# Kernel optimization log

Hardware: AMD Instinct MI355X
Metric: run time of the kernel (lower is better)

The kernel has to match this reference:

```python
import jax, jax.numpy as jnp
import numpy as np

N, E, D, H, G = 20000, 640000, 128, 128, 256  # nodes, edges, in_dim, hidden, num_graphs


def _xavier(k, shp):
    lim = float(np.sqrt(6.0 / (shp[0] + shp[1])))
    return jax.random.uniform(k, shp, jnp.float32, -lim, lim)


def setup_inputs() -> dict:
    key = jax.random.key(0)
    ks = jax.random.split(key, 16)
    x = jax.random.normal(ks[0], (N, D), jnp.float32)
    edge_index = jax.random.randint(ks[1], (2, E), 0, N)
    batch = jnp.sort(jax.random.randint(ks[2], (N,), 0, G))
    inp = {"x": x, "edge_index": edge_index, "batch": batch}
    dims = [(D, H), (H, H), (H, H)]
    ki = 3
    for i, (din, dh) in enumerate(dims):  # GIN MLP per layer: Linear-ReLU-Linear
        inp[f"w1_{i}"] = _xavier(ks[ki], (din, dh)); ki += 1
        inp[f"b1_{i}"] = jnp.zeros((dh,), jnp.float32)
        inp[f"w2_{i}"] = _xavier(ks[ki], (dh, dh)); ki += 1
        inp[f"b2_{i}"] = jnp.zeros((dh,), jnp.float32)
    inp["head_w1"] = _xavier(ks[ki], (H, H // 2)); ki += 1
    inp["head_b1"] = jnp.zeros((H // 2,), jnp.float32)
    inp["head_w2"] = _xavier(ks[ki], (H // 2, 1))
    inp["head_b2"] = jnp.zeros((1,), jnp.float32)
    return inp


def reference(x, edge_index, batch,
              w1_0, b1_0, w2_0, b2_0,
              w1_1, b1_1, w2_1, b2_1,
              w1_2, b1_2, w2_2, b2_2,
              head_w1, head_b1, head_w2, head_b2):
    src, dst = edge_index[0], edge_index[1]
    layers = [(w1_0, b1_0, w2_0, b2_0), (w1_1, b1_1, w2_1, b2_1), (w1_2, b1_2, w2_2, b2_2)]
    h = x
    for w1, b1, w2, b2 in layers:
        # GINConv (eps=0): aggregate neighbor sum + self, then MLP
        agg = jax.ops.segment_sum(h[src], dst, num_segments=N)  # [N, d] scatter-add
        z = agg + h
        z = jnp.maximum(z @ w1 + b1, 0.0) @ w2 + b2
        h = jnp.maximum(z, 0.0)  # ReLU after conv
    # global_mean_pool over graph ids
    sums = jax.ops.segment_sum(h, batch, num_segments=G)            # [G, H]
    counts = jax.ops.segment_sum(jnp.ones((N,), h.dtype), batch, num_segments=G)
    pooled = sums / jnp.maximum(counts, 1.0)[:, None]
    # head: Linear-ReLU-(Dropout eval=identity)-Linear
    hid = jnp.maximum(pooled @ head_w1 + head_b1, 0.0)
    return hid @ head_w2 + head_b2  # [G, 1]
```

## Files before the change

kernel.cpp:

```cpp
#include <hip/hip_runtime.h>


#define FEAT 128
#define CAP 128
#define SPILLCAP 4096

typedef unsigned short u16;
typedef unsigned int u32;
typedef __attribute__((ext_vector_type(8))) short bf16x8;
typedef __attribute__((ext_vector_type(4))) float f32x4;

__device__ __forceinline__ u32 f2bf(float f) {
    u32 u = __float_as_uint(f);
    return (u + 0x7FFFu + ((u >> 16) & 1u)) >> 16;
}
__device__ __forceinline__ float bf2f(u32 u) { return __uint_as_float(u << 16); }
__device__ __forceinline__ float bflo(u32 u) { return __uint_as_float(u << 16); }
__device__ __forceinline__ float bfhi(u32 u) { return __uint_as_float(u & 0xFFFF0000u); }

__device__ __forceinline__ void add8(uint4 v, float* a) {
    a[0] += bflo(v.x); a[1] += bfhi(v.x);
    a[2] += bflo(v.y); a[3] += bfhi(v.y);
    a[4] += bflo(v.z); a[5] += bfhi(v.z);
    a[6] += bflo(v.w); a[7] += bfhi(v.w);
}

__global__ __launch_bounds__(256) void cvt_x_kernel(
    const float* __restrict__ x, u16* __restrict__ xb, int total4,
    int* __restrict__ cnt, int n, int* __restrict__ spillCnt)
{
    int i = blockIdx.x * 256 + threadIdx.x;
    if (i < n) cnt[i] = 0;
    if (i == 0) *spillCnt = 0;
    if (i >= total4) return;
    float4 v = reinterpret_cast<const float4*>(x)[i];
    u32 lo = f2bf(v.x) | (f2bf(v.y) << 16);
    u32 hi = f2bf(v.z) | (f2bf(v.w) << 16);
    reinterpret_cast<uint2*>(xb)[i] = make_uint2(lo, hi);
}

struct WSet { const float* w[6]; };
__global__ __launch_bounds__(256) void cvt_wt_bounds_kernel(
    WSet ws, u16* __restrict__ outHi, u16* __restrict__ outLo,
    const int* __restrict__ batch, int* __restrict__ bnd, int n, int G)
{
    if (blockIdx.y == 6) {
        int g = blockIdx.x * 256 + threadIdx.x;
        if (g > G) return;
        int lo = 0, hi = n;
        while (lo < hi) {
            int mid = (lo + hi) >> 1;
            if (batch[mid] < g) lo = mid + 1; else hi = mid;
        }
        bnd[g] = lo;
        return;
    }
    int mat = blockIdx.y;
    const float* W = ws.w[mat];
    int i = blockIdx.x * 256 + threadIdx.x;
    int nn = i >> 7, k = i & 127;
    float f = W[(size_t)k * FEAT + nn];
    u32 hi = f2bf(f);
    u32 lo = f2bf(f - bf2f(hi));
    size_t o = (size_t)mat * FEAT * FEAT + (size_t)nn * FEAT + k;
    outHi[o] = (u16)hi;
    outLo[o] = (u16)lo;
}

__global__ __launch_bounds__(256) void csort_bucket_kernel(
    const int* __restrict__ src, const int* __restrict__ dst,
    int* __restrict__ cnt, u16* __restrict__ esrc,
    int* __restrict__ spillCnt, int2* __restrict__ spill, int nE)
{
    int e4 = (blockIdx.x * 256 + threadIdx.x) * 4;
    if (e4 + 3 < nE) {
        int4 d = *reinterpret_cast<const int4*>(&dst[e4]);
        int4 sv = *reinterpret_cast<const int4*>(&src[e4]);
        int p0 = atomicAdd(&cnt[d.x], 1);
        int p1 = atomicAdd(&cnt[d.y], 1);
        int p2 = atomicAdd(&cnt[d.z], 1);
        int p3 = atomicAdd(&cnt[d.w], 1);
        if (p0 < CAP) esrc[(size_t)d.x * CAP + p0] = (u16)sv.x;
        else { int q = atomicAdd(spillCnt, 1); if (q < SPILLCAP) spill[q] = make_int2(d.x, sv.x); }
        if (p1 < CAP) esrc[(size_t)d.y * CAP + p1] = (u16)sv.y;
        else { int q = atomicAdd(spillCnt, 1); if (q < SPILLCAP) spill[q] = make_int2(d.y, sv.y); }
        if (p2 < CAP) esrc[(size_t)d.z * CAP + p2] = (u16)sv.z;
        else { int q = atomicAdd(spillCnt, 1); if (q < SPILLCAP) spill[q] = make_int2(d.z, sv.z); }
        if (p3 < CAP) esrc[(size_t)d.w * CAP + p3] = (u16)sv.w;
        else { int q = atomicAdd(spillCnt, 1); if (q < SPILLCAP) spill[q] = make_int2(d.w, sv.w); }
    } else {
        for (int e = e4; e < nE; ++e) {
            int d = dst[e], s = src[e];
            int p = atomicAdd(&cnt[d], 1);
            if (p < CAP) esrc[(size_t)d * CAP + p] = (u16)s;
            else { int q = atomicAdd(spillCnt, 1); if (q < SPILLCAP) spill[q] = make_int2(d, s); }
        }
    }
}

__global__ __launch_bounds__(1024) void gin_layer_kernel(
    const u16* __restrict__ hin, const int* __restrict__ cnt,
    const u16* __restrict__ esrc,
    const int* __restrict__ spillCnt, const int2* __restrict__ spill,
    const u16* __restrict__ W1h, const u16* __restrict__ W1l,
    const float* __restrict__ B1,
    const u16* __restrict__ W2h, const u16* __restrict__ W2l,
    const float* __restrict__ B2,
    u16* __restrict__ out, int n)
{
    __shared__ float z_lds[4][16][132];
    __shared__ u16 thi_lds[16 * FEAT];
    __shared__ u16 tlo_lds[16 * FEAT];

    int tid = threadIdx.x;
    int rowBase = blockIdx.x * 16;

    {
        int nr = tid >> 6;
        int grp = (tid >> 4) & 3;
        int lane = tid & 15;
        int node = rowBase + nr;
        const uint4* h4 = reinterpret_cast<const uint4*>(hin);
        float a[8] = {0.f, 0.f, 0.f, 0.f, 0.f, 0.f, 0.f, 0.f};
        if (grp == 0) {
            uint4 u = h4[(size_t)node * 16 + lane];
            add8(u, a);
        }
        int len = cnt[node];
        if (len > CAP) len = CAP;
        int base = node * CAP;
        int qlen = (len + 3) >> 2;
        int gbeg = grp * qlen;
        int gend = min(gbeg + qlen, len);
        for (int j = gbeg; j < gend; j += 8) {
            uint4 v[8];
#pragma unroll
            for (int q = 0; q < 8; ++q) {
                int jj = j + q;
                int jc = jj < gend ? jj : (gend - 1);
                v[q] = h4[(size_t)esrc[base + jc] * 16 + lane];
                u32 m = (jj < gend) ? 0xFFFFFFFFu : 0u;
                v[q].x &= m; v[q].y &= m; v[q].z &= m; v[q].w &= m;
            }
#pragma unroll
            for (int q = 0; q < 8; ++q) add8(v[q], a);
        }
        if (grp == 0) {
            int sc = *spillCnt;
            if (sc > SPILLCAP) sc = SPILLCAP;
            for (int i = 0; i < sc; ++i) {
                int2 e = spill[i];
                if (e.x == node) {
                    uint4 v = h4[(size_t)e.y * 16 + lane];
                    add8(v, a);
                }
            }
        }
        *reinterpret_cast<float4*>(&z_lds[grp][nr][lane * 8]) =
            make_float4(a[0], a[1], a[2], a[3]);
        *reinterpret_cast<float4*>(&z_lds[grp][nr][lane * 8 + 4]) =
            make_float4(a[4], a[5], a[6], a[7]);
    }

    __syncthreads();

    int w = tid >> 6;
    int l = tid & 63;
    int l16 = l & 15;
    int lq = l >> 4;

    bf16x8 ah[4], al[4];
    f32x4 acc = (f32x4){0.f, 0.f, 0.f, 0.f};

    if (w < 8) {
#pragma unroll
        for (int q = 0; q < 4; ++q) {
            int off = q * 32 + lq * 8;
            float fv[8];
#pragma unroll
            for (int i = 0; i < 8; ++i) fv[i] = 0.0f;
#pragma unroll
            for (int g = 0; g < 4; ++g) {
                const float* zr = &z_lds[g][l16][off];
                float4 f0 = *reinterpret_cast<const float4*>(zr);
                float4 f1 = *reinterpret_cast<const float4*>(zr + 4);
                fv[0] += f0.x; fv[1] += f0.y; fv[2] += f0.z; fv[3] += f0.w;
                fv[4] += f1.x; fv[5] += f1.y; fv[6] += f1.z; fv[7] += f1.w;
            }
            bf16x8 hv, lv;
#pragma unroll
            for (int i = 0; i < 8; ++i) {
                u32 hb = f2bf(fv[i]);
                u32 lb = f2bf(fv[i] - bf2f(hb));
                hv[i] = (short)hb; lv[i] = (short)lb;
            }
            ah[q] = hv; al[q] = lv;
        }

        {
            const bf16x8* WrowH = reinterpret_cast<const bf16x8*>(W1h + (size_t)(w * 16 + l16) * FEAT);
            const bf16x8* WrowL = reinterpret_cast<const bf16x8*>(W1l + (size_t)(w * 16 + l16) * FEAT);
#pragma unroll
            for (int q = 0; q < 4; ++q) {
                bf16x8 wh = WrowH[q * 4 + lq];
                bf16x8 wl = WrowL[q * 4 + lq];
                acc = __builtin_amdgcn_mfma_f32_16x16x32_bf16(ah[q], wh, acc, 0, 0, 0);
                acc = __builtin_amdgcn_mfma_f32_16x16x32_bf16(al[q], wh, acc, 0, 0, 0);
                acc = __builtin_amdgcn_mfma_f32_16x16x32_bf16(ah[q], wl, acc, 0, 0, 0);
            }
        }

        {
            int col = w * 16 + l16;
            float bias = B1[col];
            int base16 = (w * 32) + ((l16 & 8) << 1);
            int fine = (l16 & 7) << 1;
#pragma unroll
            for (int r = 0; r < 4; ++r) {
                int rt = lq * 4 + r;
                float v = fmaxf(acc[r] + bias, 0.0f);
                u32 hi = f2bf(v);
                u32 lo = f2bf(v - bf2f(hi));
                int idx = (rt * 256 + ((base16 ^ (rt << 4)) | fine)) >> 1;
                thi_lds[idx] = (u16)hi;
                tlo_lds[idx] = (u16)lo;
            }
        }
    }

    __syncthreads();

    if (w < 8) {
        const bf16x8* thb = reinterpret_cast<const bf16x8*>(thi_lds);
        const bf16x8* tlb = reinterpret_cast<const bf16x8*>(tlo_lds);
        bf16x8 a2h[4], a2l[4];
#pragma unroll
        for (int q = 0; q < 4; ++q) {
            int idx = l16 * 16 + ((q * 4 + lq) ^ l16);
            a2h[q] = thb[idx];
            a2l[q] = tlb[idx];
        }

        acc = (f32x4){0.f, 0.f, 0.f, 0.f};

        {
            const bf16x8* WrowH = reinterpret_cast<const bf16x8*>(W2h + (size_t)(w * 16 + l16) * FEAT);
            const bf16x8* WrowL = reinterpret_cast<const bf16x8*>(W2l + (size_t)(w * 16 + l16) * FEAT);
#pragma unroll
            for (int q = 0; q < 4; ++q) {
                bf16x8 wh = WrowH[q * 4 + lq];
                bf16x8 wl = WrowL[q * 4 + lq];
                acc = __builtin_amdgcn_mfma_f32_16x16x32_bf16(a2h[q], wh, acc, 0, 0, 0);
                acc = __builtin_amdgcn_mfma_f32_16x16x32_bf16(a2l[q], wh, acc, 0, 0, 0);
                acc = __builtin_amdgcn_mfma_f32_16x16x32_bf16(a2h[q], wl, acc, 0, 0, 0);
            }
        }

        {
            int col = w * 16 + l16;
            float bias = B2[col];
#pragma unroll
            for (int r = 0; r < 4; ++r) {
                int m = rowBase + lq * 4 + r;
                float v = fmaxf(acc[r] + bias, 0.0f);
                out[(size_t)m * FEAT + col] = (u16)f2bf(v);
            }
        }
    }
}

__global__ __launch_bounds__(128) void pool_head_kernel(
    const u16* __restrict__ h, const int* __restrict__ bnd,
    const float* __restrict__ w1, const float* __restrict__ b1,
    const float* __restrict__ w2, const float* __restrict__ b2,
    float* __restrict__ out)
{
    int g = blockIdx.x;
    int f = threadIdx.x;
    __shared__ float p[FEAT];
    int beg = bnd[g], end = bnd[g + 1];
    float s = 0.0f;
    for (int i = beg; i < end; ++i)
        s += __uint_as_float((u32)h[(size_t)i * FEAT + f] << 16);
    float inv = (end > beg) ? 1.0f / (float)(end - beg) : 1.0f;
    p[f] = s * inv;
    __syncthreads();
    if (f < 64) {
        int j = f;
        float acc = b1[j];
#pragma unroll 8
        for (int k = 0; k < FEAT; ++k) acc = fmaf(p[k], w1[k * 64 + j], acc);
        float hid = fmaxf(acc, 0.0f);
        float prod = hid * w2[j];
#pragma unroll
        for (int off = 32; off > 0; off >>= 1) prod += __shfl_down(prod, off);
        if (j == 0) out[g] = prod + b2[0];
    }
}

extern "C" void kernel_launch(void* const* d_in, const int* in_sizes, int n_in,
                              void* d_out, int out_size, void* d_ws, size_t ws_size,
                              hipStream_t stream) {
    const float* x     = (const float*)d_in[0];
    const int*   ei    = (const int*)d_in[1];
    const int*   batch = (const int*)d_in[2];
    const float* b1[3] = {(const float*)d_in[4], (const float*)d_in[8], (const float*)d_in[12]};
    const float* b2[3] = {(const float*)d_in[6], (const float*)d_in[10], (const float*)d_in[14]};
    const float* hw1 = (const float*)d_in[15];
    const float* hb1 = (const float*)d_in[16];
    const float* hw2 = (const float*)d_in[17];
    const float* hb2 = (const float*)d_in[18];

    int N = in_sizes[0] / FEAT;
    int E = in_sizes[1] / 2;
    int G = out_size;

    u16* wtsH = (u16*)d_ws;
    u16* wtsL = wtsH + (size_t)6 * FEAT * FEAT;
    u16* xb  = wtsL + (size_t)6 * FEAT * FEAT;
    u16* hA  = xb + (size_t)N * FEAT;
    u16* hB  = hA + (size_t)N * FEAT;
    u16* esrc = hB + (size_t)N * FEAT;
    int* bnd      = (int*)(esrc + (size_t)N * CAP);
    int* cnt      = bnd + (G + 1);
    int* spillCnt = cnt + N;
    int2* spill   = (int2*)(spillCnt + 4);

    const int* src = ei;
    const int* dstv = ei + E;

    int e4Blocks = (E / 4 + 255) / 256;

    cvt_x_kernel<<<(N * FEAT / 4 + 255) / 256, 256, 0, stream>>>(
        x, xb, N * FEAT / 4, cnt, N, spillCnt);
    WSet ws;
    ws.w[0] = (const float*)d_in[3];  ws.w[1] = (const float*)d_in[5];
    ws.w[2] = (const float*)d_in[7];  ws.w[3] = (const float*)d_in[9];
    ws.w[4] = (const float*)d_in[11]; ws.w[5] = (const float*)d_in[13];
    cvt_wt_bounds_kernel<<<dim3(64, 7), 256, 0, stream>>>(ws, wtsH, wtsL, batch, bnd, N, G);

    csort_bucket_kernel<<<e4Blocks, 256, 0, stream>>>(
        src, dstv, cnt, esrc, spillCnt, spill, E);

    int layerBlocks = (N + 15) / 16;
    const u16* lin[3] = {xb, hA, hB};
    u16*       lout[3] = {hA, hB, hA};
    for (int l = 0; l < 3; ++l) {
        gin_layer_kernel<<<layerBlocks, 1024, 0, stream>>>(
            lin[l], cnt, esrc, spillCnt, spill,
            wtsH + (size_t)(2 * l) * FEAT * FEAT, wtsL + (size_t)(2 * l) * FEAT * FEAT, b1[l],
            wtsH + (size_t)(2 * l + 1) * FEAT * FEAT, wtsL + (size_t)(2 * l + 1) * FEAT * FEAT, b2[l],
            lout[l], N);
    }

    pool_head_kernel<<<G, 128, 0, stream>>>(hA, bnd, hw1, hb1, hw2, hb2, (float*)d_out);
}
```

Baseline: 203.3 us.

## Halve GIN layer block to 512 threads and stage edge lists in LDS

The layer kernel now runs 512 threads per block. Each node's neighbours are gathered by two 16-lane groups instead of four, and all 8 waves do the MLP work, so no waves sit idle during the matmul phase. The block's 16 rows of the padded edge-source table are first copied into LDS with one coalesced load, so the gather reads indices from LDS rather than global memory. In exchange, each group gathers twice as many neighbours serially, and there is an extra barrier plus a fixed 4KB copy even for short edge lists.

```diff
diff --git a/kernel.cpp b/kernel.cpp
--- a/kernel.cpp
+++ b/kernel.cpp
@@ -98,7 +98,7 @@
     }
 }
 
-__global__ __launch_bounds__(1024) void gin_layer_kernel(
+__global__ __launch_bounds__(512) void gin_layer_kernel(
     const u16* __restrict__ hin, const int* __restrict__ cnt,
     const u16* __restrict__ esrc,
     const int* __restrict__ spillCnt, const int2* __restrict__ spill,
@@ -108,16 +108,22 @@
     const float* __restrict__ B2,
     u16* __restrict__ out, int n)
 {
-    __shared__ float z_lds[4][16][132];
+    __shared__ float z_lds[2][16][132];
+    __shared__ u16 e_lds[16 * CAP];
     __shared__ u16 thi_lds[16 * FEAT];
     __shared__ u16 tlo_lds[16 * FEAT];
 
     int tid = threadIdx.x;
     int rowBase = blockIdx.x * 16;
 
-    {
-        int nr = tid >> 6;
-        int grp = (tid >> 4) & 3;
+    reinterpret_cast<uint2*>(e_lds)[tid] =
+        reinterpret_cast<const uint2*>(esrc)[(size_t)rowBase * (CAP / 4) + tid];
+
+    __syncthreads();
+
+    {
+        int nr = tid >> 5;
+        int grp = (tid >> 4) & 1;
         int lane = tid & 15;
         int node = rowBase + nr;
         const uint4* h4 = reinterpret_cast<const uint4*>(hin);
@@ -128,17 +134,17 @@
         }
         int len = cnt[node];
         if (len > CAP) len = CAP;
-        int base = node * CAP;
-        int qlen = (len + 3) >> 2;
-        int gbeg = grp * qlen;
-        int gend = min(gbeg + qlen, len);
+        int half = (len + 1) >> 1;
+        int gbeg = grp * half;
+        int gend = grp ? len : half;
+        const u16* eb = &e_lds[nr * CAP];
         for (int j = gbeg; j < gend; j += 8) {
             uint4 v[8];
 #pragma unroll
             for (int q = 0; q < 8; ++q) {
                 int jj = j + q;
                 int jc = jj < gend ? jj : (gend - 1);
-                v[q] = h4[(size_t)esrc[base + jc] * 16 + lane];
+                v[q] = h4[(size_t)eb[jc] * 16 + lane];
                 u32 m = (jj < gend) ? 0xFFFFFFFFu : 0u;
                 v[q].x &= m; v[q].y &= m; v[q].z &= m; v[q].w &= m;
             }
@@ -170,101 +176,93 @@
     int lq = l >> 4;
 
     bf16x8 ah[4], al[4];
+#pragma unroll
+    for (int q = 0; q < 4; ++q) {
+        const float* zr0 = &z_lds[0][l16][q * 32 + lq * 8];
+        const float* zr1 = &z_lds[1][l16][q * 32 + lq * 8];
+        float4 f0 = *reinterpret_cast<const float4*>(zr0);
+        float4 f1 = *reinterpret_cast<const float4*>(zr0 + 4);
+        float4 g0 = *reinterpret_cast<const float4*>(zr1);
+        float4 g1 = *reinterpret_cast<const float4*>(zr1 + 4);
+        float fv[8] = {f0.x + g0.x, f0.y + g0.y, f0.z + g0.z, f0.w + g0.w,
+                       f1.x + g1.x, f1.y + g1.y, f1.z + g1.z, f1.w + g1.w};
+        bf16x8 hv, lv;
+#pragma unroll
+        for (int i = 0; i < 8; ++i) {
+            u32 hb = f2bf(fv[i]);
+            u32 lb = f2bf(fv[i] - bf2f(hb));
+            hv[i] = (short)hb; lv[i] = (short)lb;
+        }
+        ah[q] = hv; al[q] = lv;
+    }
+
     f32x4 acc = (f32x4){0.f, 0.f, 0.f, 0.f};
 
-    if (w < 8) {
+    {
+        const bf16x8* WrowH = reinterpret_cast<const bf16x8*>(W1h + (size_t)(w * 16 + l16) * FEAT);
+        const bf16x8* WrowL = reinterpret_cast<const bf16x8*>(W1l + (size_t)(w * 16 + l16) * FEAT);
 #pragma unroll
         for (int q = 0; q < 4; ++q) {
-            int off = q * 32 + lq * 8;
-            float fv[8];
-#pragma unroll
-            for (int i = 0; i < 8; ++i) fv[i] = 0.0f;
-#pragma unroll
-            for (int g = 0; g < 4; ++g) {
-                const float* zr = &z_lds[g][l16][off];
-                float4 f0 = *reinterpret_cast<const float4*>(zr);
-                float4 f1 = *reinterpret_cast<const float4*>(zr + 4);
-                fv[0] += f0.x; fv[1] += f0.y; fv[2] += f0.z; fv[3] += f0.w;
-                fv[4] += f1.x; fv[5] += f1.y; fv[6] += f1.z; fv[7] += f1.w;
-            }
-            bf16x8 hv, lv;
-#pragma unroll
-            for (int i = 0; i < 8; ++i) {
-                u32 hb = f2bf(fv[i]);
-                u32 lb = f2bf(fv[i] - bf2f(hb));
-                hv[i] = (short)hb; lv[i] = (short)lb;
-            }
-            ah[q] = hv; al[q] = lv;
-        }
-
-        {
-            const bf16x8* WrowH = reinterpret_cast<const bf16x8*>(W1h + (size_t)(w * 16 + l16) * FEAT);
-            const bf16x8* WrowL = reinterpret_cast<const bf16x8*>(W1l + (size_t)(w * 16 + l16) * FEAT);
-#pragma unroll
-            for (int q = 0; q < 4; ++q) {
-                bf16x8 wh = WrowH[q * 4 + lq];
-                bf16x8 wl = WrowL[q * 4 + lq];
-                acc = __builtin_amdgcn_mfma_f32_16x16x32_bf16(ah[q], wh, acc, 0, 0, 0);
-                acc = __builtin_amdgcn_mfma_f32_16x16x32_bf16(al[q], wh, acc, 0, 0, 0);
-                acc = __builtin_amdgcn_mfma_f32_16x16x32_bf16(ah[q], wl, acc, 0, 0, 0);
-            }
-        }
-
-        {
-            int col = w * 16 + l16;
-            float bias = B1[col];
-            int base16 = (w * 32) + ((l16 & 8) << 1);
-            int fine = (l16 & 7) << 1;
-#pragma unroll
-            for (int r = 0; r < 4; ++r) {
-                int rt = lq * 4 + r;
-                float v = fmaxf(acc[r] + bias, 0.0f);
-                u32 hi = f2bf(v);
-                u32 lo = f2bf(v - bf2f(hi));
-                int idx = (rt * 256 + ((base16 ^ (rt << 4)) | fine)) >> 1;
-                thi_lds[idx] = (u16)hi;
-                tlo_lds[idx] = (u16)lo;
-            }
+            bf16x8 wh = WrowH[q * 4 + lq];
+            bf16x8 wl = WrowL[q * 4 + lq];
+            acc = __builtin_amdgcn_mfma_f32_16x16x32_bf16(ah[q], wh, acc, 0, 0, 0);
+            acc = __builtin_amdgcn_mfma_f32_16x16x32_bf16(al[q], wh, acc, 0, 0, 0);
+            acc = __builtin_amdgcn_mfma_f32_16x16x32_bf16(ah[q], wl, acc, 0, 0, 0);
+        }
+    }
+
+    {
+        int col = w * 16 + l16;
+        float bias = B1[col];
+        int base16 = (w * 32) + ((l16 & 8) << 1);
+        int fine = (l16 & 7) << 1;
+#pragma unroll
+        for (int r = 0; r < 4; ++r) {
+            int rt = lq * 4 + r;
+            float v = fmaxf(acc[r] + bias, 0.0f);
+            u32 hi = f2bf(v);
+            u32 lo = f2bf(v - bf2f(hi));
+            int idx = (rt * 256 + ((base16 ^ (rt << 4)) | fine)) >> 1;
+            thi_lds[idx] = (u16)hi;
+            tlo_lds[idx] = (u16)lo;
         }
     }
 
     __syncthreads();
 
-    if (w < 8) {
-        const bf16x8* thb = reinterpret_cast<const bf16x8*>(thi_lds);
-        const bf16x8* tlb = reinterpret_cast<const bf16x8*>(tlo_lds);
-        bf16x8 a2h[4], a2l[4];
+    const bf16x8* thb = reinterpret_cast<const bf16x8*>(thi_lds);
+    const bf16x8* tlb = reinterpret_cast<const bf16x8*>(tlo_lds);
+    bf16x8 a2h[4], a2l[4];
+#pragma unroll
+    for (int q = 0; q < 4; ++q) {
+        int idx = l16 * 16 + ((q * 4 + lq) ^ l16);
+        a2h[q] = thb[idx];
+        a2l[q] = tlb[idx];
+    }
+
+    acc = (f32x4){0.f, 0.f, 0.f, 0.f};
+
+    {
+        const bf16x8* WrowH = reinterpret_cast<const bf16x8*>(W2h + (size_t)(w * 16 + l16) * FEAT);
+        const bf16x8* WrowL = reinterpret_cast<const bf16x8*>(W2l + (size_t)(w * 16 + l16) * FEAT);
 #pragma unroll
         for (int q = 0; q < 4; ++q) {
-            int idx = l16 * 16 + ((q * 4 + lq) ^ l16);
-            a2h[q] = thb[idx];
-            a2l[q] = tlb[idx];
-        }
-
-        acc = (f32x4){0.f, 0.f, 0.f, 0.f};
-
-        {
-            const bf16x8* WrowH = reinterpret_cast<const bf16x8*>(W2h + (size_t)(w * 16 + l16) * FEAT);
-            const bf16x8* WrowL = reinterpret_cast<const bf16x8*>(W2l + (size_t)(w * 16 + l16) * FEAT);
-#pragma unroll
-            for (int q = 0; q < 4; ++q) {
-                bf16x8 wh = WrowH[q * 4 + lq];
-                bf16x8 wl = WrowL[q * 4 + lq];
-                acc = __builtin_amdgcn_mfma_f32_16x16x32_bf16(a2h[q], wh, acc, 0, 0, 0);
-                acc = __builtin_amdgcn_mfma_f32_16x16x32_bf16(a2l[q], wh, acc, 0, 0, 0);
-                acc = __builtin_amdgcn_mfma_f32_16x16x32_bf16(a2h[q], wl, acc, 0, 0, 0);
-            }
-        }
-
-        {
-            int col = w * 16 + l16;
-            float bias = B2[col];
-#pragma unroll
-            for (int r = 0; r < 4; ++r) {
-                int m = rowBase + lq * 4 + r;
-                float v = fmaxf(acc[r] + bias, 0.0f);
-                out[(size_t)m * FEAT + col] = (u16)f2bf(v);
-            }
+            bf16x8 wh = WrowH[q * 4 + lq];
+            bf16x8 wl = WrowL[q * 4 + lq];
+            acc = __builtin_amdgcn_mfma_f32_16x16x32_bf16(a2h[q], wh, acc, 0, 0, 0);
+            acc = __builtin_amdgcn_mfma_f32_16x16x32_bf16(a2l[q], wh, acc, 0, 0, 0);
+            acc = __builtin_amdgcn_mfma_f32_16x16x32_bf16(a2h[q], wl, acc, 0, 0, 0);
+        }
+    }
+
+    {
+        int col = w * 16 + l16;
+        float bias = B2[col];
+#pragma unroll
+        for (int r = 0; r < 4; ++r) {
+            int m = rowBase + lq * 4 + r;
+            float v = fmaxf(acc[r] + bias, 0.0f);
+            out[(size_t)m * FEAT + col] = (u16)f2bf(v);
         }
     }
 }
@@ -346,7 +344,7 @@
     const u16* lin[3] = {xb, hA, hB};
     u16*       lout[3] = {hA, hB, hA};
     for (int l = 0; l < 3; ++l) {
-        gin_layer_kernel<<<layerBlocks, 1024, 0, stream>>>(
+        gin_layer_kernel<<<layerBlocks, 512, 0, stream>>>(
             lin[l], cnt, esrc, spillCnt, spill,
             wtsH + (size_t)(2 * l) * FEAT * FEAT, wtsL + (size_t)(2 * l) * FEAT * FEAT, b1[l],
             wtsH + (size_t)(2 * l + 1) * FEAT * FEAT, wtsL + (size_t)(2 * l + 1) * FEAT * FEAT, b2[l],
```

Result: faster. 173.1 us (median of 2 runs) (-14.9%).
